# Performance work log

Measured on AMD Instinct MI355X. Metric: run time of the kernel, lower is better.

Reference implementation:

```python
import jax, jax.numpy as jnp
import numpy as np

B, S, HID, NH = 2, 2048, 2048, 16
HD = HID // NH  # head_dim = 128


def setup_inputs() -> dict:
    key = jax.random.key(0)
    ks = jax.random.split(key, 10)
    sc = 1.0 / np.sqrt(HID)
    inp = {
        "hidden_state": jax.random.normal(ks[0], (B, S, HID), dtype=jnp.float32),
        # upper-triangular (strict) causal mask: 1 where attention is forbidden
        "casual_mask": jnp.triu(jnp.ones((S, S), dtype=jnp.float32), k=1),
        # pad last 128 tokens of each sequence
        "pad_mask": jnp.concatenate(
            [jnp.zeros((B, S - 128), jnp.float32), jnp.ones((B, 128), jnp.float32)], axis=1
        ),
        # weights stored [in, out] (transposed vs torch Linear)
        "Wq": jax.random.normal(ks[1], (HID, HID), dtype=jnp.float32) * sc,
        "bq": jnp.zeros((HID,), jnp.float32),
        "Wk": jax.random.normal(ks[2], (HID, HD), dtype=jnp.float32) * sc,
        "bk": jnp.zeros((HD,), jnp.float32),
        "Wv": jax.random.normal(ks[3], (HID, HD), dtype=jnp.float32) * sc,
        "bv": jnp.zeros((HD,), jnp.float32),
        "Wo": jax.random.normal(ks[4], (HID, HID), dtype=jnp.float32) * sc,
        "bo": jnp.zeros((HID,), jnp.float32),
    }
    return inp


def reference(hidden_state, casual_mask, pad_mask, Wq, bq, Wk, bk, Wv, bv, Wo, bo):
    bsz, seq_len, hid = hidden_state.shape
    nh = NH
    hd = hid // nh
    q = hidden_state @ Wq + bq                      # [B,S,HID]
    k = hidden_state @ Wk + bk                      # [B,S,HD]  single shared head
    v = hidden_state @ Wv + bv                      # [B,S,HD]
    q = q.reshape(bsz, seq_len, nh, hd).transpose(0, 2, 1, 3)  # [B,NH,S,HD]
    # attn scores: shared K broadcast across all query heads
    scores = jnp.einsum("bhqd,bkd->bhqk", q, k) / jnp.sqrt(jnp.float32(hd))
    scores = scores + casual_mask * (-1e9)
    scores = scores + pad_mask[:, None, None, :] * (-1e9)
    probs = jax.nn.softmax(scores, axis=-1)         # [B,NH,S,S]
    out = jnp.einsum("bhqk,bkd->bhqd", probs, v)    # [B,NH,S,HD]
    out = out.transpose(0, 2, 1, 3).reshape(bsz, seq_len, hid)
    return out @ Wo + bo
```

## Files before the change

kernel.cpp:

```cpp
#include <hip/hip_runtime.h>
#include <hip/hip_bf16.h>
#include <math.h>

#define B_    2
#define S_    2048
#define HID_  2048
#define NH_   16
#define HD_   128
#define MTOT  4096
#define QKV_N 2304

typedef short bf16x8 __attribute__((ext_vector_type(8)));
typedef float f32x4  __attribute__((ext_vector_type(4)));
typedef float f32x16 __attribute__((ext_vector_type(16)));

__device__ __forceinline__ ushort f2bf(float f) {
    __hip_bfloat16 h = __float2bfloat16(f);
    ushort u; __builtin_memcpy(&u, &h, 2); return u;
}

__device__ __forceinline__ uint cvtpk_bf16(float lo, float hi) {
    uint r;
    asm("v_cvt_pk_bf16_f32 %0, %1, %2" : "=v"(r) : "v"(lo), "v"(hi));
    return r;
}

__device__ __forceinline__ void gload_lds16(const void* g, void* l) {
    __builtin_amdgcn_global_load_lds(
        (const __attribute__((address_space(1))) void*)g,
        (__attribute__((address_space(3))) void*)l, 16, 0, 0);
}

__global__ void cast_f32_bf16(const float* __restrict__ in, ushort* __restrict__ out)
{
    long i = ((long)blockIdx.x * 256 + threadIdx.x) * 8;
    float4 a = *(const float4*)&in[i];
    float4 b = *(const float4*)&in[i + 4];
    uint4 o;
    o.x = (uint)f2bf(a.x) | ((uint)f2bf(a.y) << 16);
    o.y = (uint)f2bf(a.z) | ((uint)f2bf(a.w) << 16);
    o.z = (uint)f2bf(b.x) | ((uint)f2bf(b.y) << 16);
    o.w = (uint)f2bf(b.z) | ((uint)f2bf(b.w) << 16);
    *(uint4*)&out[i] = o;
}

__global__ void transcast(const float* __restrict__ W, ushort* __restrict__ T,
                          int N, int rowoff)
{
    __shared__ float tile[32][33];
    const int tx = threadIdx.x & 31, ty = threadIdx.x >> 5;
    const int n0 = blockIdx.x * 32, k0 = blockIdx.y * 32;
#pragma unroll
    for (int i = 0; i < 4; i++)
        tile[ty + 8 * i][tx] = W[(long)(k0 + ty + 8 * i) * N + n0 + tx];
    __syncthreads();
#pragma unroll
    for (int i = 0; i < 4; i++)
        T[(long)(rowoff + n0 + ty + 8 * i) * 2048 + k0 + tx] = f2bf(tile[tx][ty + 8 * i]);
}

__global__ void fuse_bias(const float* __restrict__ bq, const float* __restrict__ bk,
                          const float* __restrict__ bv, float* __restrict__ bqkv)
{
    int i = blockIdx.x * 256 + threadIdx.x;
    if (i < 2048)      bqkv[i] = bq[i];
    else if (i < 2176) bqkv[i] = bk[i - 2048];
    else if (i < QKV_N) bqkv[i] = bv[i - 2176];
}

__global__ __launch_bounds__(256, 2) void gemm_qkv(
    const ushort* __restrict__ A, const ushort* __restrict__ Bt,
    const float* __restrict__ bias,
    ushort* __restrict__ qbuf, ushort* __restrict__ kbuf,
    ushort* __restrict__ vtbuf)
{
    const int K = HID_;
    __shared__ __align__(16) ushort As[128 * 32];
    __shared__ __align__(16) ushort Bs[128 * 32];
    const int t = threadIdx.x;
    const int w = t >> 6, l = t & 63;
    const long bm = (long)blockIdx.y * 128;
    const long bn = (long)blockIdx.x * 128;

    f32x4 acc[4][4];
#pragma unroll
    for (int i = 0; i < 4; i++)
#pragma unroll
        for (int j = 0; j < 4; j++) acc[i][j] = (f32x4){0.f, 0.f, 0.f, 0.f};

    const int srow = w * 16 + (l >> 2);
    const int scol = (l & 3) * 8;
    const ushort* Ag0 = A + (bm + srow) * (long)K + scol;
    const ushort* Ag1 = A + (bm + srow + 64) * (long)K + scol;
    const ushort* Bg0 = Bt + (bn + srow) * (long)K + scol;
    const ushort* Bg1 = Bt + (bn + srow + 64) * (long)K + scol;
    ushort* Al0 = As + w * 512;
    ushort* Al1 = As + 2048 + w * 512;
    ushort* Bl0 = Bs + w * 512;
    ushort* Bl1 = Bs + 2048 + w * 512;

    const int mrow = l & 15, kq = l >> 4;
    const int moff = (w & 1) * 64, noff = (w >> 1) * 64;

    for (int k0 = 0; k0 < K; k0 += 32) {
        gload_lds16(Ag0 + k0, Al0);
        gload_lds16(Ag1 + k0, Al1);
        gload_lds16(Bg0 + k0, Bl0);
        gload_lds16(Bg1 + k0, Bl1);
        __syncthreads();
        bf16x8 af[4], bfr[4];
#pragma unroll
        for (int i = 0; i < 4; i++)
            af[i] = *(const bf16x8*)&As[(moff + i * 16 + mrow) * 32 + kq * 8];
#pragma unroll
        for (int j = 0; j < 4; j++)
            bfr[j] = *(const bf16x8*)&Bs[(noff + j * 16 + mrow) * 32 + kq * 8];
#pragma unroll
        for (int i = 0; i < 4; i++)
#pragma unroll
            for (int j = 0; j < 4; j++)
                acc[i][j] = __builtin_amdgcn_mfma_f32_16x16x32_bf16(
                    af[i], bfr[j], acc[i][j], 0, 0, 0);
        __syncthreads();
    }

    const int crow = (l >> 4) * 4, ccol = l & 15;
    const int tile = blockIdx.x;
#pragma unroll
    for (int i = 0; i < 4; i++) {
#pragma unroll
        for (int j = 0; j < 4; j++) {
            long colg = bn + noff + j * 16 + ccol;
            float bv = bias[colg];
            long row0 = bm + moff + i * 16 + crow;
            float v[4];
#pragma unroll
            for (int r = 0; r < 4; r++) v[r] = acc[i][j][r] + bv;
            if (tile < 16) {
#pragma unroll
                for (int r = 0; r < 4; r++)
                    qbuf[(row0 + r) * (long)HID_ + colg] = f2bf(v[r]);
            } else if (tile == 16) {
                long ck = colg - 2048;
#pragma unroll
                for (int r = 0; r < 4; r++)
                    kbuf[(row0 + r) * (long)HD_ + ck] = f2bf(v[r]);
            } else {
                long cv = colg - 2176;
                long b  = row0 >> 11;
                long s0 = row0 & 2047;
                ushort4 pk;
                pk.x = f2bf(v[0]); pk.y = f2bf(v[1]);
                pk.z = f2bf(v[2]); pk.w = f2bf(v[3]);
                *(ushort4*)&vtbuf[b * (HD_ * (long)S_) + cv * (long)S_ + s0] = pk;
            }
        }
    }
}

__global__ __launch_bounds__(256, 2) void gemm_mfma(
    const ushort* __restrict__ A, const ushort* __restrict__ Bt,
    const float* __restrict__ bias, float* __restrict__ C,
    int K, int ldc)
{
    __shared__ __align__(16) ushort As[128 * 32];
    __shared__ __align__(16) ushort Bs[128 * 32];
    const int t = threadIdx.x;
    const int w = t >> 6, l = t & 63;
    const long bm = (long)blockIdx.y * 128;
    const long bn = (long)blockIdx.x * 128;

    f32x4 acc[4][4];
#pragma unroll
    for (int i = 0; i < 4; i++)
#pragma unroll
        for (int j = 0; j < 4; j++) acc[i][j] = (f32x4){0.f, 0.f, 0.f, 0.f};

    const int srow = w * 16 + (l >> 2);
    const int scol = (l & 3) * 8;
    const ushort* Ag0 = A + (bm + srow) * (long)K + scol;
    const ushort* Ag1 = A + (bm + srow + 64) * (long)K + scol;
    const ushort* Bg0 = Bt + (bn + srow) * (long)K + scol;
    const ushort* Bg1 = Bt + (bn + srow + 64) * (long)K + scol;
    ushort* Al0 = As + w * 512;
    ushort* Al1 = As + 2048 + w * 512;
    ushort* Bl0 = Bs + w * 512;
    ushort* Bl1 = Bs + 2048 + w * 512;

    const int mrow = l & 15, kq = l >> 4;
    const int moff = (w & 1) * 64, noff = (w >> 1) * 64;

    for (int k0 = 0; k0 < K; k0 += 32) {
        gload_lds16(Ag0 + k0, Al0);
        gload_lds16(Ag1 + k0, Al1);
        gload_lds16(Bg0 + k0, Bl0);
        gload_lds16(Bg1 + k0, Bl1);
        __syncthreads();
        bf16x8 af[4], bfr[4];
#pragma unroll
        for (int i = 0; i < 4; i++)
            af[i] = *(const bf16x8*)&As[(moff + i * 16 + mrow) * 32 + kq * 8];
#pragma unroll
        for (int j = 0; j < 4; j++)
            bfr[j] = *(const bf16x8*)&Bs[(noff + j * 16 + mrow) * 32 + kq * 8];
#pragma unroll
        for (int i = 0; i < 4; i++)
#pragma unroll
            for (int j = 0; j < 4; j++)
                acc[i][j] = __builtin_amdgcn_mfma_f32_16x16x32_bf16(
                    af[i], bfr[j], acc[i][j], 0, 0, 0);
        __syncthreads();
    }

    const int crow = (l >> 4) * 4, ccol = l & 15;
#pragma unroll
    for (int i = 0; i < 4; i++) {
#pragma unroll
        for (int j = 0; j < 4; j++) {
            long col = bn + noff + j * 16 + ccol;
            float bv = bias[col];
#pragma unroll
            for (int r = 0; r < 4; r++) {
                long row = bm + moff + i * 16 + crow + r;
                C[row * (long)ldc + col] = acc[i][j][r] + bv;
            }
        }
    }
}

__global__ __launch_bounds__(512, 2) void attn_mfma(
    const ushort* __restrict__ qbuf, const ushort* __restrict__ kbuf,
    const ushort* __restrict__ vtbuf, ushort* __restrict__ outp)
{
    __shared__ __align__(16) char smem[69632];
    ushort* KsB  = (ushort*)smem;
    ushort* VtB  = (ushort*)(smem + 32768);

    const int h = blockIdx.y, b = blockIdx.z;
    const int t = threadIdx.x, w = t >> 6, l = t & 63;
    const int l31 = l & 31, h5 = l >> 5;
    const long rowbase = (long)b * S_;

    const int qblkA = 15 - (int)blockIdx.x;
    const int qblkB = (int)blockIdx.x;
    const int myqblk = (w >> 2) ? qblkB : qblkA;
    const int wq = w & 3;
    const int qbase = myqblk * 128 + wq * 32;
    const int qmaxw = qbase + 31;
    const int kTiles = 2 * qblkA + 2;

    const ushort* kg[2]; int klo[2];
    const ushort* vg[2]; int vlo[2];
#pragma unroll
    for (int i = 0; i < 2; i++) {
        const int c = w * 2 + i;
        int key0 = c * 4 + (l >> 4);
        int gk = (l & 15) ^ (key0 & 15);
        kg[i] = kbuf + (rowbase + key0) * (long)HD_ + gk * 8;
        klo[i] = (c * 4) * 128 + l * 8;
        int d = c * 8 + (l >> 3);
        int gv = (l & 7) ^ (d & 7);
        vg[i] = vtbuf + ((long)b * HD_ + d) * (long)S_ + gv * 8;
        vlo[i] = (c * 8) * 64 + l * 8;
    }

    bf16x8 qf[8];
    {
        const ushort* qp = qbuf + (rowbase + qbase + l31) * (long)HID_
                                + h * HD_ + h5 * 8;
#pragma unroll
        for (int ks = 0; ks < 8; ks++) qf[ks] = *(const bf16x8*)(qp + ks * 16);
    }

    f32x16 o[4] = {};
    float mrun = -1e30f, lrun = 0.f;

    const float SC = 0.08838834764831845f * 1.44269504089f;

#pragma unroll
    for (int i = 0; i < 2; i++) {
        gload_lds16(kg[i], KsB + klo[i]);
        gload_lds16(vg[i], VtB + vlo[i]);
    }
    __syncthreads();

    for (int kt = 0; kt < kTiles; kt++) {
        const int cur = kt & 1;
        const int ktb = kt * 64;

        if (kt + 1 < kTiles) {
            const int nxt = cur ^ 1;
            const long nb = (long)(ktb + 64);
#pragma unroll
            for (int i = 0; i < 2; i++) {
                gload_lds16(kg[i] + nb * HD_, KsB + nxt * 8192 + klo[i]);
                gload_lds16(vg[i] + nb, VtB + nxt * 8192 + vlo[i]);
            }
        }

        if (ktb <= qmaxw) {
            const ushort* Ks = KsB + cur * 8192;
            const ushort* Vt = VtB + cur * 8192;

            f32x16 c[2] = {};
#pragma unroll
            for (int mb = 0; mb < 2; mb++) {
                const int key = mb * 32 + l31;
#pragma unroll
                for (int ks = 0; ks < 8; ks++) {
                    int g = (ks * 2 + h5) ^ (key & 15);
                    bf16x8 a = *(const bf16x8*)&Ks[key * 128 + g * 8];
                    c[mb] = __builtin_amdgcn_mfma_f32_32x32x16_bf16(
                        a, qf[ks], c[mb], 0, 0, 0);
                }
            }

            const bool boundary = (ktb + 63 > qbase) || (ktb >= S_ - 128);
            if (boundary) {
                const int qg = qbase + l31;
#pragma unroll
                for (int mb = 0; mb < 2; mb++)
#pragma unroll
                    for (int g = 0; g < 4; g++)
#pragma unroll
                        for (int r = 0; r < 4; r++) {
                            int key = ktb + mb * 32 + 4 * h5 + 8 * g + r;
                            if (key > qg || key >= S_ - 128)
                                c[mb][g * 4 + r] = -3.0e38f;
                        }
            }

            float a0 = -3.0e38f, a1 = -3.0e38f, a2 = -3.0e38f, a3 = -3.0e38f;
#pragma unroll
            for (int mb = 0; mb < 2; mb++)
#pragma unroll
                for (int g = 0; g < 4; g++) {
                    a0 = fmaxf(a0, c[mb][g * 4 + 0]);
                    a1 = fmaxf(a1, c[mb][g * 4 + 1]);
                    a2 = fmaxf(a2, c[mb][g * 4 + 2]);
                    a3 = fmaxf(a3, c[mb][g * 4 + 3]);
                }
            float vmax = fmaxf(fmaxf(a0, a1), fmaxf(a2, a3));
            vmax = fmaxf(vmax, __shfl_xor(vmax, 32));
            const float vmaxs = vmax * SC;

            if (!__all(vmaxs <= mrun + 8.0f)) {
                float mnew  = fmaxf(mrun, vmaxs);
                float alpha = __builtin_amdgcn_exp2f(mrun - mnew);
#pragma unroll
                for (int mb = 0; mb < 4; mb++) o[mb] *= alpha;
                lrun *= alpha;
                mrun = mnew;
            }

            float s0 = 0.f, s1 = 0.f, s2 = 0.f, s3 = 0.f;
#pragma unroll
            for (int mb = 0; mb < 2; mb++)
#pragma unroll
                for (int g = 0; g < 4; g++) {
                    float p0 = __builtin_amdgcn_exp2f(__builtin_fmaf(c[mb][g * 4 + 0], SC, -mrun));
                    float p1 = __builtin_amdgcn_exp2f(__builtin_fmaf(c[mb][g * 4 + 1], SC, -mrun));
                    float p2 = __builtin_amdgcn_exp2f(__builtin_fmaf(c[mb][g * 4 + 2], SC, -mrun));
                    float p3 = __builtin_amdgcn_exp2f(__builtin_fmaf(c[mb][g * 4 + 3], SC, -mrun));
                    c[mb][g * 4 + 0] = p0; s0 += p0;
                    c[mb][g * 4 + 1] = p1; s1 += p1;
                    c[mb][g * 4 + 2] = p2; s2 += p2;
                    c[mb][g * 4 + 3] = p3; s3 += p3;
                }
            float sum = (s0 + s1) + (s2 + s3);
            sum += __shfl_xor(sum, 32);
            lrun += sum;

#pragma unroll
            for (int ks2 = 0; ks2 < 4; ks2++) {
                const int mbs = ks2 >> 1;
                const int base = (ks2 & 1) * 8;
                uint X = cvtpk_bf16(c[mbs][base + 0], c[mbs][base + 1]);
                uint Y = cvtpk_bf16(c[mbs][base + 2], c[mbs][base + 3]);
                uint Z = cvtpk_bf16(c[mbs][base + 4], c[mbs][base + 5]);
                uint Wd = cvtpk_bf16(c[mbs][base + 6], c[mbs][base + 7]);
                asm("v_permlane32_swap_b32 %0, %1" : "+v"(X), "+v"(Z));
                asm("v_permlane32_swap_b32 %0, %1" : "+v"(Y), "+v"(Wd));
                uint tmp[4] = {X, Y, Z, Wd};
                bf16x8 pf;
                __builtin_memcpy(&pf, tmp, 16);
#pragma unroll
                for (int mb = 0; mb < 4; mb++) {
                    int d = mb * 32 + l31;
                    int g = (ks2 * 2 + h5) ^ (d & 7);
                    bf16x8 a = *(const bf16x8*)&Vt[d * 64 + g * 8];
                    o[mb] = __builtin_amdgcn_mfma_f32_32x32x16_bf16(
                        a, pf, o[mb], 0, 0, 0);
                }
            }
        }
        __syncthreads();
    }

    ushort* Ob = (ushort*)smem + w * 4352;
    float inv = 1.f / lrun;
#pragma unroll
    for (int mb = 0; mb < 4; mb++) {
#pragma unroll
        for (int g = 0; g < 4; g++) {
            int d0 = mb * 32 + 4 * h5 + 8 * g;
            ushort4 pk;
            pk.x = f2bf(o[mb][g * 4 + 0] * inv);
            pk.y = f2bf(o[mb][g * 4 + 1] * inv);
            pk.z = f2bf(o[mb][g * 4 + 2] * inv);
            pk.w = f2bf(o[mb][g * 4 + 3] * inv);
            *(ushort4*)&Ob[l31 * 136 + d0] = pk;
        }
    }
    __builtin_amdgcn_s_waitcnt(0);
    {
        const int q = l >> 1, half = l & 1;
        const ushort* src = Ob + q * 136 + half * 64;
        ushort* dst = outp + (rowbase + myqblk * 128 + wq * 32 + q) * (long)HID_
                           + h * HD_ + half * 64;
#pragma unroll
        for (int i = 0; i < 8; i++) {
            uint4 v = *(const uint4*)(src + i * 8);
            *(uint4*)(dst + i * 8) = v;
        }
    }
}

extern "C" void kernel_launch(void* const* d_in, const int* in_sizes, int n_in,
                              void* d_out, int out_size, void* d_ws, size_t ws_size,
                              hipStream_t stream)
{
    const float* hidden = (const float*)d_in[0];
    const float* Wq  = (const float*)d_in[3];
    const float* bq  = (const float*)d_in[4];
    const float* Wk  = (const float*)d_in[5];
    const float* bk  = (const float*)d_in[6];
    const float* Wv  = (const float*)d_in[7];
    const float* bv  = (const float*)d_in[8];
    const float* Wo  = (const float*)d_in[9];
    const float* bo  = (const float*)d_in[10];
    float* out = (float*)d_out;

    char* ws = (char*)d_ws;
    ushort* hbf   = (ushort*)(ws);
    ushort* WqkvT = (ushort*)(ws + 16777216);
    ushort* WoT   = (ushort*)(ws + 26214400);
    float*  bqkv  = (float*) (ws + 34603008);
    ushort* qbuf  = (ushort*)(ws + 34619392);
    ushort* kbuf  = (ushort*)(ws + 51396608);
    ushort* vtbuf = (ushort*)(ws + 52445184);
    ushort* attnO = (ushort*)(ws + 53493760);

    cast_f32_bf16<<<4096, 256, 0, stream>>>(hidden, hbf);
    transcast<<<dim3(64, 64), 256, 0, stream>>>(Wq, WqkvT, 2048, 0);
    transcast<<<dim3(4, 64),  256, 0, stream>>>(Wk, WqkvT, 128, 2048);
    transcast<<<dim3(4, 64),  256, 0, stream>>>(Wv, WqkvT, 128, 2176);
    transcast<<<dim3(64, 64), 256, 0, stream>>>(Wo, WoT, 2048, 0);
    fuse_bias<<<9, 256, 0, stream>>>(bq, bk, bv, bqkv);

    gemm_qkv<<<dim3(18, 32), 256, 0, stream>>>(hbf, WqkvT, bqkv,
                                               qbuf, kbuf, vtbuf);
    attn_mfma<<<dim3(8, NH_, B_), 512, 0, stream>>>(qbuf, kbuf, vtbuf, attnO);
    gemm_mfma<<<dim3(16, 32), 256, 0, stream>>>(attnO, WoT, bo, out,
                                                HID_, HID_);
}
```

Before: 305.3 us.

## Double-buffer GEMM LDS tiles and split attention into single-qblock 256-thread blocks

Both GEMM kernels now hold two LDS stages and prefetch the next K tile while computing the current one, which removes the load-then-barrier stall at the top of each iteration. The attention kernel moves from 512-thread blocks, each pairing a short and a long causal query block, to 256-thread blocks that each own one query block. A 1-D grid orders the blocks so they are spread across heads and batches, and each wave now stages four K/V chunks instead of two. This doubles GEMM LDS use and gives attention blocks uneven causal work, so occupancy and load balance could suffer.

```diff
diff --git a/kernel.cpp b/kernel.cpp
--- a/kernel.cpp
+++ b/kernel.cpp
@@ -75,8 +75,8 @@
     ushort* __restrict__ vtbuf)
 {
     const int K = HID_;
-    __shared__ __align__(16) ushort As[128 * 32];
-    __shared__ __align__(16) ushort Bs[128 * 32];
+    __shared__ __align__(16) ushort As[2 * 128 * 32];
+    __shared__ __align__(16) ushort Bs[2 * 128 * 32];
     const int t = threadIdx.x;
     const int w = t >> 6, l = t & 63;
     const long bm = (long)blockIdx.y * 128;
@@ -102,19 +102,29 @@
     const int mrow = l & 15, kq = l >> 4;
     const int moff = (w & 1) * 64, noff = (w >> 1) * 64;
 
+    gload_lds16(Ag0, Al0);
+    gload_lds16(Ag1, Al1);
+    gload_lds16(Bg0, Bl0);
+    gload_lds16(Bg1, Bl1);
+    __syncthreads();
+
     for (int k0 = 0; k0 < K; k0 += 32) {
-        gload_lds16(Ag0 + k0, Al0);
-        gload_lds16(Ag1 + k0, Al1);
-        gload_lds16(Bg0 + k0, Bl0);
-        gload_lds16(Bg1 + k0, Bl1);
-        __syncthreads();
+        const int cb = (k0 >> 5) & 1;
+        const int po = cb * 4096;
+        if (k0 + 32 < K) {
+            const int pn = (cb ^ 1) * 4096;
+            gload_lds16(Ag0 + k0 + 32, Al0 + pn);
+            gload_lds16(Ag1 + k0 + 32, Al1 + pn);
+            gload_lds16(Bg0 + k0 + 32, Bl0 + pn);
+            gload_lds16(Bg1 + k0 + 32, Bl1 + pn);
+        }
         bf16x8 af[4], bfr[4];
 #pragma unroll
         for (int i = 0; i < 4; i++)
-            af[i] = *(const bf16x8*)&As[(moff + i * 16 + mrow) * 32 + kq * 8];
+            af[i] = *(const bf16x8*)&As[po + (moff + i * 16 + mrow) * 32 + kq * 8];
 #pragma unroll
         for (int j = 0; j < 4; j++)
-            bfr[j] = *(const bf16x8*)&Bs[(noff + j * 16 + mrow) * 32 + kq * 8];
+            bfr[j] = *(const bf16x8*)&Bs[po + (noff + j * 16 + mrow) * 32 + kq * 8];
 #pragma unroll
         for (int i = 0; i < 4; i++)
 #pragma unroll
@@ -163,8 +173,8 @@
     const float* __restrict__ bias, float* __restrict__ C,
     int K, int ldc)
 {
-    __shared__ __align__(16) ushort As[128 * 32];
-    __shared__ __align__(16) ushort Bs[128 * 32];
+    __shared__ __align__(16) ushort As[2 * 128 * 32];
+    __shared__ __align__(16) ushort Bs[2 * 128 * 32];
     const int t = threadIdx.x;
     const int w = t >> 6, l = t & 63;
     const long bm = (long)blockIdx.y * 128;
@@ -190,19 +200,29 @@
     const int mrow = l & 15, kq = l >> 4;
     const int moff = (w & 1) * 64, noff = (w >> 1) * 64;
 
+    gload_lds16(Ag0, Al0);
+    gload_lds16(Ag1, Al1);
+    gload_lds16(Bg0, Bl0);
+    gload_lds16(Bg1, Bl1);
+    __syncthreads();
+
     for (int k0 = 0; k0 < K; k0 += 32) {
-        gload_lds16(Ag0 + k0, Al0);
-        gload_lds16(Ag1 + k0, Al1);
-        gload_lds16(Bg0 + k0, Bl0);
-        gload_lds16(Bg1 + k0, Bl1);
-        __syncthreads();
+        const int cb = (k0 >> 5) & 1;
+        const int po = cb * 4096;
+        if (k0 + 32 < K) {
+            const int pn = (cb ^ 1) * 4096;
+            gload_lds16(Ag0 + k0 + 32, Al0 + pn);
+            gload_lds16(Ag1 + k0 + 32, Al1 + pn);
+            gload_lds16(Bg0 + k0 + 32, Bl0 + pn);
+            gload_lds16(Bg1 + k0 + 32, Bl1 + pn);
+        }
         bf16x8 af[4], bfr[4];
 #pragma unroll
         for (int i = 0; i < 4; i++)
-            af[i] = *(const bf16x8*)&As[(moff + i * 16 + mrow) * 32 + kq * 8];
+            af[i] = *(const bf16x8*)&As[po + (moff + i * 16 + mrow) * 32 + kq * 8];
 #pragma unroll
         for (int j = 0; j < 4; j++)
-            bfr[j] = *(const bf16x8*)&Bs[(noff + j * 16 + mrow) * 32 + kq * 8];
+            bfr[j] = *(const bf16x8*)&Bs[po + (noff + j * 16 + mrow) * 32 + kq * 8];
 #pragma unroll
         for (int i = 0; i < 4; i++)
 #pragma unroll
@@ -228,32 +248,32 @@
     }
 }
 
-__global__ __launch_bounds__(512, 2) void attn_mfma(
+__global__ __launch_bounds__(256, 2) void attn_mfma(
     const ushort* __restrict__ qbuf, const ushort* __restrict__ kbuf,
     const ushort* __restrict__ vtbuf, ushort* __restrict__ outp)
 {
-    __shared__ __align__(16) char smem[69632];
+    __shared__ __align__(16) char smem[65536];
     ushort* KsB  = (ushort*)smem;
     ushort* VtB  = (ushort*)(smem + 32768);
 
-    const int h = blockIdx.y, b = blockIdx.z;
+    const int bx = blockIdx.x;
+    const int qblk = (bx < 256) ? (bx >> 5) : (15 - ((bx - 256) >> 5));
+    const int hb = bx & 31;
+    const int h = hb & 15, b = hb >> 4;
+
     const int t = threadIdx.x, w = t >> 6, l = t & 63;
     const int l31 = l & 31, h5 = l >> 5;
     const long rowbase = (long)b * S_;
 
-    const int qblkA = 15 - (int)blockIdx.x;
-    const int qblkB = (int)blockIdx.x;
-    const int myqblk = (w >> 2) ? qblkB : qblkA;
-    const int wq = w & 3;
-    const int qbase = myqblk * 128 + wq * 32;
+    const int qbase = qblk * 128 + w * 32;
     const int qmaxw = qbase + 31;
-    const int kTiles = 2 * qblkA + 2;
-
-    const ushort* kg[2]; int klo[2];
-    const ushort* vg[2]; int vlo[2];
-#pragma unroll
-    for (int i = 0; i < 2; i++) {
-        const int c = w * 2 + i;
+    const int kTiles = 2 * qblk + 2;
+
+    const ushort* kg[4]; int klo[4];
+    const ushort* vg[4]; int vlo[4];
+#pragma unroll
+    for (int i = 0; i < 4; i++) {
+        const int c = w * 4 + i;
         int key0 = c * 4 + (l >> 4);
         int gk = (l & 15) ^ (key0 & 15);
         kg[i] = kbuf + (rowbase + key0) * (long)HD_ + gk * 8;
@@ -278,7 +298,7 @@
     const float SC = 0.08838834764831845f * 1.44269504089f;
 
 #pragma unroll
-    for (int i = 0; i < 2; i++) {
+    for (int i = 0; i < 4; i++) {
         gload_lds16(kg[i], KsB + klo[i]);
         gload_lds16(vg[i], VtB + vlo[i]);
     }
@@ -292,7 +312,7 @@
             const int nxt = cur ^ 1;
             const long nb = (long)(ktb + 64);
 #pragma unroll
-            for (int i = 0; i < 2; i++) {
+            for (int i = 0; i < 4; i++) {
                 gload_lds16(kg[i] + nb * HD_, KsB + nxt * 8192 + klo[i]);
                 gload_lds16(vg[i] + nb, VtB + nxt * 8192 + vlo[i]);
             }
@@ -416,7 +436,7 @@
     {
         const int q = l >> 1, half = l & 1;
         const ushort* src = Ob + q * 136 + half * 64;
-        ushort* dst = outp + (rowbase + myqblk * 128 + wq * 32 + q) * (long)HID_
+        ushort* dst = outp + (rowbase + qblk * 128 + w * 32 + q) * (long)HID_
                            + h * HD_ + half * 64;
 #pragma unroll
         for (int i = 0; i < 8; i++) {
@@ -460,7 +480,7 @@
 
     gemm_qkv<<<dim3(18, 32), 256, 0, stream>>>(hbf, WqkvT, bqkv,
                                                qbuf, kbuf, vtbuf);
-    attn_mfma<<<dim3(8, NH_, B_), 512, 0, stream>>>(qbuf, kbuf, vtbuf, attnO);
+    attn_mfma<<<512, 256, 0, stream>>>(qbuf, kbuf, vtbuf, attnO);
     gemm_mfma<<<dim3(16, 32), 256, 0, stream>>>(attnO, WoT, bo, out,
                                                 HID_, HID_);
 }
```

Measured after the change: 298.7 us. 1.02x faster.
